# Kernel optimization log

Hardware: AMD Instinct MI355X
Metric: run time of the kernel (lower is better)

## Reference

```python
import jax, jax.numpy as jnp
import numpy as np

B, D_IN, D_H = 8192, 1024, 1024


def setup_inputs() -> dict:
    key = jax.random.key(0)
    ks = jax.random.split(key, 11)
    s_in = 1.0 / np.sqrt(D_IN)
    s_h = 1.0 / np.sqrt(D_H)
    return {
        "x": jax.random.normal(ks[0], (B, D_IN), jnp.float32),
        "h": jax.random.normal(ks[1], (B, D_H), jnp.float32),
        "Wiz": jax.random.normal(ks[2], (D_IN, D_H), jnp.float32) * s_in,
        "Uhz": jax.random.normal(ks[3], (D_H, D_H), jnp.float32) * s_h,
        "bz": jax.random.normal(ks[4], (D_H,), jnp.float32) * 0.01,
        "Wir": jax.random.normal(ks[5], (D_IN, D_H), jnp.float32) * s_in,
        "Uhr": jax.random.normal(ks[6], (D_H, D_H), jnp.float32) * s_h,
        "br": jax.random.normal(ks[7], (D_H,), jnp.float32) * 0.01,
        "Win": jax.random.normal(ks[8], (D_IN, D_H), jnp.float32) * s_in,
        "Uhn": jax.random.normal(ks[9], (D_H, D_H), jnp.float32) * s_h,
        "bn": jax.random.normal(ks[10], (D_H,), jnp.float32) * 0.01,
    }


def reference(x, h, Wiz, Uhz, bz, Wir, Uhr, br, Win, Uhn, bn):
    # Concatenate input-side weights into one GEMM for efficiency; math identical.
    Wi = jnp.concatenate([Wiz, Wir, Win], axis=1)          # [D_in, 3H]
    xz, xr, xn = jnp.split(x @ Wi, 3, axis=1)              # each [B, H]
    Uh = jnp.concatenate([Uhz, Uhr], axis=1)               # [H, 2H]
    hz, hr = jnp.split(h @ Uh, 2, axis=1)
    z = jax.nn.sigmoid(xz + hz + bz)
    r = jax.nn.sigmoid(xr + hr + br)
    # Faithful to source: (r * h) @ Uhn, and act1 (sigmoid) for n, not tanh.
    n = jax.nn.sigmoid(xn + (r * h) @ Uhn + bn)
    return (1.0 - z) * h + z * n
```

## Files before the change

### kernel.cpp

```cpp
#include <hip/hip_runtime.h>
#include <hip/hip_bf16.h>

typedef __attribute__((ext_vector_type(8))) short short8;
typedef __attribute__((ext_vector_type(4))) float f32x4;

#define DEV __device__ __forceinline__

DEV float bf2f(unsigned short u) {
    union { unsigned int i; float f; } v;
    v.i = ((unsigned int)u) << 16;
    return v.f;
}
DEV unsigned short f2bf(float f) {
    union { float f; unsigned int i; } v; v.f = f;
    unsigned int r = v.i + 0x7FFFu + ((v.i >> 16) & 1u);
    return (unsigned short)(r >> 16);
}
DEV float sigmoidf_(float x) {
    return 1.0f / (1.0f + __expf(-x));
}

__global__ void conv_xh(const float* __restrict__ x, const float* __restrict__ h,
                        unsigned short* __restrict__ xw, unsigned short* __restrict__ hw,
                        int n)
{
    int i = (blockIdx.x * blockDim.x + threadIdx.x) * 8;
    const float* src; unsigned short* dst; int off;
    if (i < n) { src = x; dst = xw; off = i; }
    else       { src = h; dst = hw; off = i - n; }
    float4 a = *(const float4*)(src + off);
    float4 b = *(const float4*)(src + off + 4);
    union { uint4 v; unsigned short s[8]; } o;
    o.s[0]=f2bf(a.x); o.s[1]=f2bf(a.y); o.s[2]=f2bf(a.z); o.s[3]=f2bf(a.w);
    o.s[4]=f2bf(b.x); o.s[5]=f2bf(b.y); o.s[6]=f2bf(b.z); o.s[7]=f2bf(b.w);
    *(uint4*)(dst + off) = o.v;
}

__global__ void tconv(const float* __restrict__ Wiz, const float* __restrict__ Uhz,
                      const float* __restrict__ Wir, const float* __restrict__ Uhr,
                      const float* __restrict__ Win, const float* __restrict__ Uhn,
                      unsigned short* __restrict__ B1t, unsigned short* __restrict__ B3t)
{
    __shared__ float lds[32][33];
    const float* src; unsigned short* dst;
    switch (blockIdx.z) {
        case 0: src=Wiz; dst=B1t;                            break;
        case 1: src=Uhz; dst=B1t + 1024;                     break;
        case 2: src=Wir; dst=B1t + (size_t)1024*2048;        break;
        case 3: src=Uhr; dst=B1t + (size_t)1024*2048 + 1024; break;
        case 4: src=Win; dst=B3t;                            break;
        default: src=Uhn; dst=B3t + 1024;                    break;
    }
    int k0 = blockIdx.x * 32, n0 = blockIdx.y * 32;
    int tx = threadIdx.x & 31, ty = threadIdx.x >> 5;
    #pragma unroll
    for (int i = 0; i < 4; i++)
        lds[ty + 8*i][tx] = src[(size_t)(k0 + ty + 8*i)*1024 + n0 + tx];
    __syncthreads();
    #pragma unroll
    for (int i = 0; i < 4; i++)
        dst[(size_t)(n0 + ty + 8*i)*2048 + k0 + tx] = f2bf(lds[tx][ty + 8*i]);
}

template<int EPI>
__global__ __launch_bounds__(256, 2)
void gemm_bt(const unsigned short* __restrict__ A0,
             const unsigned short* __restrict__ A1,
             const unsigned short* __restrict__ Bt,
             const float* __restrict__ bias0,
             const float* __restrict__ bias1,
             const float* __restrict__ hsrc,
             float* __restrict__ zbuf,
             unsigned short* __restrict__ rh,
             float* __restrict__ out)
{
    __shared__ unsigned short lA[128*32];
    __shared__ unsigned short lB[128*32];
    const int tid = threadIdx.x;
    const int gm = blockIdx.x * 128, gn = blockIdx.y * 128;

    const int w  = tid >> 6, l = tid & 63;
    const int wm = (w >> 1) * 64, wn = (w & 1) * 64;
    const int lr = l & 15, lk = l >> 4;

    f32x4 acc[4][4] = {};

    const int srow = tid >> 2;
    const int scol = (tid & 3) * 8;
    char* lAp = (char*)lA + tid * 16;
    char* lBp = (char*)lB + tid * 16;

    for (int kt = 0; kt < 2048; kt += 32) {
        const unsigned short* Ab = (kt < 1024 ? A0 : A1)
                                 + (size_t)(gm + srow) * 1024 + (kt & 1023) + scol;
        const unsigned short* Bb = Bt + (size_t)(gn + srow) * 2048 + kt + scol;
        __syncthreads();
        __builtin_amdgcn_global_load_lds(
            (const __attribute__((address_space(1))) void*)Ab,
            (__attribute__((address_space(3))) void*)lAp, 16, 0, 0);
        __builtin_amdgcn_global_load_lds(
            (const __attribute__((address_space(1))) void*)(Ab + (size_t)64*1024),
            (__attribute__((address_space(3))) void*)(lAp + 4096), 16, 0, 0);
        __builtin_amdgcn_global_load_lds(
            (const __attribute__((address_space(1))) void*)Bb,
            (__attribute__((address_space(3))) void*)lBp, 16, 0, 0);
        __builtin_amdgcn_global_load_lds(
            (const __attribute__((address_space(1))) void*)(Bb + (size_t)64*2048),
            (__attribute__((address_space(3))) void*)(lBp + 4096), 16, 0, 0);
        __syncthreads();

        short8 af[4], bfr[4];
        #pragma unroll
        for (int mi = 0; mi < 4; mi++)
            af[mi] = *(const short8*)&lA[(wm + mi*16 + lr)*32 + lk*8];
        #pragma unroll
        for (int ni = 0; ni < 4; ni++)
            bfr[ni] = *(const short8*)&lB[(wn + ni*16 + lr)*32 + lk*8];
        #pragma unroll
        for (int mi = 0; mi < 4; mi++)
            #pragma unroll
            for (int ni = 0; ni < 4; ni++)
                acc[mi][ni] = __builtin_amdgcn_mfma_f32_16x16x32_bf16(
                    af[mi], bfr[ni], acc[mi][ni], 0, 0, 0);
    }

    #pragma unroll
    for (int mi = 0; mi < 4; mi++) {
        #pragma unroll
        for (int j = 0; j < 4; j++) {
            int row = gm + wm + mi*16 + lk*4 + j;
            #pragma unroll
            for (int ni = 0; ni < 4; ni++) {
                int col = gn + wn + ni*16 + lr;
                float v = acc[mi][ni][j];
                if (EPI == 1) {
                    if (col < 1024) {
                        zbuf[(size_t)row*1024 + col] = sigmoidf_(v + bias0[col]);
                    } else {
                        int c = col - 1024;
                        float rv = sigmoidf_(v + bias1[c]);
                        rh[(size_t)row*1024 + c] =
                            f2bf(rv * hsrc[(size_t)row*1024 + c]);
                    }
                } else {
                    float nv = sigmoidf_(v + bias0[col]);
                    float zv = zbuf[(size_t)row*1024 + col];
                    float hv = hsrc[(size_t)row*1024 + col];
                    out[(size_t)row*1024 + col] = (1.0f - zv)*hv + zv*nv;
                }
            }
        }
    }
}

extern "C" void kernel_launch(void* const* d_in, const int* in_sizes, int n_in,
                              void* d_out, int out_size, void* d_ws, size_t ws_size,
                              hipStream_t stream)
{
    const float* x   = (const float*)d_in[0];
    const float* h   = (const float*)d_in[1];
    const float* Wiz = (const float*)d_in[2];
    const float* Uhz = (const float*)d_in[3];
    const float* bz  = (const float*)d_in[4];
    const float* Wir = (const float*)d_in[5];
    const float* Uhr = (const float*)d_in[6];
    const float* br  = (const float*)d_in[7];
    const float* Win = (const float*)d_in[8];
    const float* Uhn = (const float*)d_in[9];
    const float* bn  = (const float*)d_in[10];
    float* out = (float*)d_out;

    char* ws = (char*)d_ws;
    const size_t MB = 1024ull * 1024ull;
    unsigned short* xw   = (unsigned short*)(ws + 0);
    unsigned short* hw   = (unsigned short*)(ws + 16*MB);
    unsigned short* B1t  = (unsigned short*)(ws + 32*MB);
    unsigned short* B3t  = (unsigned short*)(ws + 40*MB);
    float*          zbuf = (float*)(ws + 44*MB);
    unsigned short* rh   = (unsigned short*)(ws + 76*MB);

    const int B = 8192, H = 1024;

    conv_xh<<<dim3(2*B*H/8/256), dim3(256), 0, stream>>>(x, h, xw, hw, B*H);

    tconv<<<dim3(32, 32, 6), dim3(256), 0, stream>>>(
        Wiz, Uhz, Wir, Uhr, Win, Uhn, B1t, B3t);

    gemm_bt<1><<<dim3(64, 16), dim3(256), 0, stream>>>(
        xw, hw, B1t, bz, br, h, zbuf, rh, nullptr);

    gemm_bt<2><<<dim3(64, 8), dim3(256), 0, stream>>>(
        xw, rh, B3t, bn, nullptr, h, zbuf, nullptr, out);
}
```

Before: 293.5 us.

## Replace first GRU GEMM with 256x256 8-wave double-buffered phased kernel

Rewrites the first (z/r gate) GEMM as a 512-thread kernel with 256x256 tiles, K-tile 64 and double-buffered 128KB dynamic LDS. Global-to-LDS loads for future tiles are interleaved with the MFMA phases, using explicit waitcnt, barriers and setprio. Block IDs are remapped for better L2 locality. The aim is to hide memory latency and raise MFMA utilisation over the old single-buffer 128x128 kernel, at the cost of heavy LDS use (likely one block per CU despite launch_bounds 2) and fragile hand-written synchronisation. The second GEMM is only specialised.

```diff
diff --git a/kernel.cpp b/kernel.cpp
--- a/kernel.cpp
+++ b/kernel.cpp
@@ -62,17 +62,161 @@
         dst[(size_t)(n0 + ty + 8*i)*2048 + k0 + tx] = f2bf(lds[tx][ty + 8*i]);
 }
 
-template<int EPI>
+DEV void stage_band_A(char* smem, const unsigned short* A0, const unsigned short* A1,
+                      int buf, int band, int ktile, int gm, int tid)
+{
+    const unsigned short* src = (ktile < 16) ? A0 : A1;
+    int kofs = (ktile & 15) * 64;
+    #pragma unroll
+    for (int j = 0; j < 2; ++j) {
+        int o  = tid * 16 + j * 8192;
+        int rp = o >> 7;
+        int k  = (o & 127) >> 1;
+        int m  = ((rp >> 6) << 7) | (band << 6) | (rp & 63);
+        const unsigned short* g = src + (size_t)(gm + m) * 1024 + kofs + k;
+        __builtin_amdgcn_global_load_lds(
+            (const __attribute__((address_space(1))) void*)g,
+            (__attribute__((address_space(3))) void*)(smem + buf*32768 + band*16384 + o),
+            16, 0, 0);
+    }
+}
+DEV void stage_band_B(char* smem, const unsigned short* Bt,
+                      int buf, int band, int ktile, int gn, int tid)
+{
+    #pragma unroll
+    for (int j = 0; j < 2; ++j) {
+        int o  = tid * 16 + j * 8192;
+        int rp = o >> 7;
+        int k  = (o & 127) >> 1;
+        int n  = ((rp >> 5) << 6) | (band << 5) | (rp & 31);
+        const unsigned short* g = Bt + (size_t)(gn + n) * 2048 + ktile * 64 + k;
+        __builtin_amdgcn_global_load_lds(
+            (const __attribute__((address_space(1))) void*)g,
+            (__attribute__((address_space(3))) void*)(smem + 65536 + buf*32768 + band*16384 + o),
+            16, 0, 0);
+    }
+}
+
+#define LOAD_A(BUF,MH)                                                        \
+    { _Pragma("unroll") for (int mi = 0; mi < 4; mi++)                        \
+      { _Pragma("unroll") for (int ks = 0; ks < 2; ks++)                      \
+        af[mi][ks] = *(const short8*)(smem + (BUF)*32768 + (MH)*16384         \
+                                      + abase + mi*2048 + ks*64); } }
+#define LOAD_B(BUF,NH,DST)                                                    \
+    { _Pragma("unroll") for (int ni = 0; ni < 2; ni++)                        \
+      { _Pragma("unroll") for (int ks = 0; ks < 2; ks++)                      \
+        DST[ni][ks] = *(const short8*)(smem + (BUF)*32768 + (NH)*16384        \
+                                       + bbase + ni*2048 + ks*64); } }
+#define MM(MH,NH,BF)                                                          \
+    { _Pragma("unroll") for (int mi = 0; mi < 4; mi++)                        \
+      { _Pragma("unroll") for (int ni = 0; ni < 2; ni++)                      \
+        { _Pragma("unroll") for (int ks = 0; ks < 2; ks++)                    \
+          acc[(MH)*4+mi][(NH)*2+ni] = __builtin_amdgcn_mfma_f32_16x16x32_bf16(\
+              af[mi][ks], BF[ni][ks], acc[(MH)*4+mi][(NH)*2+ni], 0, 0, 0); } } }
+#define PH_MID(DO_VM)                                                         \
+    if (DO_VM) asm volatile("s_waitcnt vmcnt(6)" ::: "memory");               \
+    __builtin_amdgcn_s_barrier();                                             \
+    asm volatile("s_waitcnt lgkmcnt(0)" ::: "memory");                        \
+    __builtin_amdgcn_s_setprio(1);
+#define PH_END                                                                \
+    __builtin_amdgcn_s_setprio(0);                                            \
+    __builtin_amdgcn_s_barrier();
+
+__global__ __launch_bounds__(512, 2)
+void gemm1_8ph(const unsigned short* __restrict__ A0,
+               const unsigned short* __restrict__ A1,
+               const unsigned short* __restrict__ Bt,
+               const float* __restrict__ bz, const float* __restrict__ br,
+               const float* __restrict__ hsrc,
+               float* __restrict__ zbuf, unsigned short* __restrict__ rh)
+{
+    extern __shared__ char smem[];
+    const int tid = threadIdx.x;
+
+    int wg = (blockIdx.x & 7) * 32 + (blockIdx.x >> 3);
+    const int gm = (wg & 31) * 256;
+    const int gn = (wg >> 5) * 256;
+
+    const int w  = tid >> 6, l = tid & 63;
+    const int wr = w >> 2, wc = w & 3;
+    const int lr = l & 15, lk = l >> 4;
+
+    const int abase = wr*8192 + lr*128 + lk*16;
+    const int bbase = 65536 + wc*4096 + lr*128 + lk*16;
+
+    f32x4 acc[8][4] = {};
+    short8 af[4][2], bf0[2][2], bf1[2][2];
+
+    stage_band_A(smem, A0, A1, 0, 0, 0, gm, tid);
+    stage_band_A(smem, A0, A1, 0, 1, 0, gm, tid);
+    stage_band_B(smem, Bt, 0, 0, 0, gn, tid);
+    stage_band_B(smem, Bt, 0, 1, 0, gn, tid);
+    stage_band_A(smem, A0, A1, 1, 0, 1, gm, tid);
+    stage_band_B(smem, Bt, 1, 0, 1, gn, tid);
+    stage_band_B(smem, Bt, 1, 1, 1, gn, tid);
+    asm volatile("s_waitcnt vmcnt(6)" ::: "memory");
+    __builtin_amdgcn_s_barrier();
+
+    for (int it = 0; it < 16; ++it) {
+        const int T  = 2 * it;
+        const int t1 = (T+1 < 31) ? T+1 : 31;
+        const int t2 = (T+2 < 31) ? T+2 : 31;
+        const int t3 = (T+3 < 31) ? T+3 : 31;
+
+        LOAD_A(0,0); LOAD_B(0,0,bf0);
+        stage_band_A(smem, A0, A1, 1, 1, t1, gm, tid);
+        PH_MID(false); MM(0,0,bf0); PH_END;
+        LOAD_B(0,1,bf1);
+        stage_band_A(smem, A0, A1, 0, 0, t2, gm, tid);
+        PH_MID(false); MM(0,1,bf1); PH_END;
+        LOAD_A(0,1);
+        stage_band_B(smem, Bt, 0, 0, t2, gn, tid);
+        PH_MID(false); MM(1,0,bf0); PH_END;
+        stage_band_B(smem, Bt, 0, 1, t2, gn, tid);
+        PH_MID(true); MM(1,1,bf1); PH_END;
+
+        LOAD_A(1,0); LOAD_B(1,0,bf0);
+        stage_band_A(smem, A0, A1, 0, 1, t2, gm, tid);
+        PH_MID(false); MM(0,0,bf0); PH_END;
+        LOAD_B(1,1,bf1);
+        stage_band_A(smem, A0, A1, 1, 0, t3, gm, tid);
+        PH_MID(false); MM(0,1,bf1); PH_END;
+        LOAD_A(1,1);
+        stage_band_B(smem, Bt, 1, 0, t3, gn, tid);
+        PH_MID(false); MM(1,0,bf0); PH_END;
+        stage_band_B(smem, Bt, 1, 1, t3, gn, tid);
+        PH_MID(true); MM(1,1,bf1); PH_END;
+    }
+
+    #pragma unroll
+    for (int Mi = 0; Mi < 8; Mi++) {
+        #pragma unroll
+        for (int j = 0; j < 4; j++) {
+            int row = gm + wr*128 + Mi*16 + lk*4 + j;
+            #pragma unroll
+            for (int Ni = 0; Ni < 4; Ni++) {
+                int col = gn + wc*64 + Ni*16 + lr;
+                float v = acc[Mi][Ni][j];
+                if (col < 1024) {
+                    zbuf[(size_t)row*1024 + col] = sigmoidf_(v + bz[col]);
+                } else {
+                    int c = col - 1024;
+                    float rv = sigmoidf_(v + br[c]);
+                    rh[(size_t)row*1024 + c] = f2bf(rv * hsrc[(size_t)row*1024 + c]);
+                }
+            }
+        }
+    }
+}
+
 __global__ __launch_bounds__(256, 2)
-void gemm_bt(const unsigned short* __restrict__ A0,
-             const unsigned short* __restrict__ A1,
-             const unsigned short* __restrict__ Bt,
-             const float* __restrict__ bias0,
-             const float* __restrict__ bias1,
-             const float* __restrict__ hsrc,
-             float* __restrict__ zbuf,
-             unsigned short* __restrict__ rh,
-             float* __restrict__ out)
+void gemm2_m97(const unsigned short* __restrict__ A0,
+               const unsigned short* __restrict__ A1,
+               const unsigned short* __restrict__ Bt,
+               const float* __restrict__ bn,
+               const float* __restrict__ hsrc,
+               const float* __restrict__ zbuf,
+               float* __restrict__ out)
 {
     __shared__ unsigned short lA[128*32];
     __shared__ unsigned short lB[128*32];
@@ -132,22 +276,10 @@
             #pragma unroll
             for (int ni = 0; ni < 4; ni++) {
                 int col = gn + wn + ni*16 + lr;
-                float v = acc[mi][ni][j];
-                if (EPI == 1) {
-                    if (col < 1024) {
-                        zbuf[(size_t)row*1024 + col] = sigmoidf_(v + bias0[col]);
-                    } else {
-                        int c = col - 1024;
-                        float rv = sigmoidf_(v + bias1[c]);
-                        rh[(size_t)row*1024 + c] =
-                            f2bf(rv * hsrc[(size_t)row*1024 + c]);
-                    }
-                } else {
-                    float nv = sigmoidf_(v + bias0[col]);
-                    float zv = zbuf[(size_t)row*1024 + col];
-                    float hv = hsrc[(size_t)row*1024 + col];
-                    out[(size_t)row*1024 + col] = (1.0f - zv)*hv + zv*nv;
-                }
+                float nv = sigmoidf_(acc[mi][ni][j] + bn[col]);
+                float zv = zbuf[(size_t)row*1024 + col];
+                float hv = hsrc[(size_t)row*1024 + col];
+                out[(size_t)row*1024 + col] = (1.0f - zv)*hv + zv*nv;
             }
         }
     }
@@ -181,14 +313,17 @@
 
     const int B = 8192, H = 1024;
 
+    (void)hipFuncSetAttribute((const void*)gemm1_8ph,
+                              hipFuncAttributeMaxDynamicSharedMemorySize, 131072);
+
     conv_xh<<<dim3(2*B*H/8/256), dim3(256), 0, stream>>>(x, h, xw, hw, B*H);
 
     tconv<<<dim3(32, 32, 6), dim3(256), 0, stream>>>(
         Wiz, Uhz, Wir, Uhr, Win, Uhn, B1t, B3t);
 
-    gemm_bt<1><<<dim3(64, 16), dim3(256), 0, stream>>>(
-        xw, hw, B1t, bz, br, h, zbuf, rh, nullptr);
-
-    gemm_bt<2><<<dim3(64, 8), dim3(256), 0, stream>>>(
-        xw, rh, B3t, bn, nullptr, h, zbuf, nullptr, out);
-}
+    gemm1_8ph<<<dim3(256), dim3(512), 131072, stream>>>(
+        xw, hw, B1t, bz, br, h, zbuf, rh);
+
+    gemm2_m97<<<dim3(64, 8), dim3(256), 0, stream>>>(
+        xw, rh, B3t, bn, h, zbuf, out);
+}
```

Measured after the change: 312.3 us. 1.06x slower.
